# Optimization experiments

Measured on AMD Instinct MI355X. Metric: run time of the kernel, lower is better.

Reference implementation:

```python
import jax, jax.numpy as jnp
import numpy as np

N_CODES = 4096
D = 256


def setup_inputs() -> dict:
    key = jax.random.key(0)
    k_v, k_w = jax.random.split(key)
    v = jax.random.normal(k_v, (8, 2048, D), dtype=jnp.float32)
    # Embedding init ~ N(0,1), then softmax over dim=1, then row 0 set to 1/d (empty feature)
    w = jax.random.normal(k_w, (N_CODES, D), dtype=jnp.float32)
    w = jax.nn.softmax(w, axis=1)
    w = w.at[0].set(1.0 / D)
    return {"v": v, "vectors": w}


def reference(v, vectors):
    n, d = vectors.shape
    cb = vectors[1:]  # exclude the fixed empty feature at index 0
    # ||v - c||^2 = ||v||^2 - 2 v.c + ||c||^2  (avoids [..., n, d] intermediate)
    v2 = jnp.sum(v * v, axis=-1, keepdims=True)              # [..., 1]
    c2 = jnp.sum(cb * cb, axis=-1)                           # [n-1]
    diff = v2 - 2.0 * jnp.einsum('...d,nd->...n', v, cb) + c2  # [..., n-1]
    idx = jnp.argmin(diff, axis=-1) + 1                      # [...]
    # empty-feature mask: any component differs from 1/d
    mask = jnp.any(v != (1.0 / d), axis=-1)
    idx = jnp.where(mask, idx, 0)
    out = vectors[idx]                                       # gather == onehot @ vectors
    loss = jnp.mean(jnp.square(out - jax.lax.stop_gradient(v)))
    used = jnp.array(0, dtype=jnp.int32)  # eval mode: usage pool is empty
    return out, idx, loss, used
```

## Files before the change

kernel.cpp:

```cpp
#include <hip/hip_runtime.h>
#include <hip/hip_fp16.h>
#include <math.h>
#include <stdint.h>


#define M_TOTAL 16384
#define NCODES  4096
#define D_DIM   256

#define OUT_OFF_IDX  (M_TOTAL * D_DIM)
#define OUT_OFF_LOSS (OUT_OFF_IDX + M_TOTAL)

#define VPLANE (M_TOTAL * D_DIM)

typedef _Float16 half8 __attribute__((ext_vector_type(8)));
typedef float    float16v __attribute__((ext_vector_type(16)));

__global__ __launch_bounds__(256) void prep_kernel(
    const float* __restrict__ V, const float* __restrict__ W,
    _Float16* __restrict__ Vhi, _Float16* __restrict__ Vlo,
    _Float16* __restrict__ Bp, float* __restrict__ v2, float* __restrict__ c2,
    uint64_t* __restrict__ pk)
{
  __shared__ float T[16 * 264];
  const int t = threadIdx.x;
  const int rloc = t >> 4, seg = t & 15;
  const bool isW = blockIdx.x < 256;
  const int bid2 = isW ? blockIdx.x : (blockIdx.x - 256);
  const int row = bid2 * 16 + rloc;
  const float* X = isW ? W : V;

  if (!isW && bid2 < 64) pk[bid2 * 256 + t] = ~0ULL;

  const float* src = X + (size_t)row * D_DIM + seg * 16;
  float4 x[4];
#pragma unroll
  for (int u = 0; u < 4; ++u) x[u] = ((const float4*)src)[u];
  union { half8 v; _Float16 e[8]; } uh[2], ul[2];
#pragma unroll
  for (int u = 0; u < 4; ++u) {
    float e4[4] = {x[u].x, x[u].y, x[u].z, x[u].w};
#pragma unroll
    for (int j = 0; j < 4; ++j) {
      const int e = u * 4 + j;
      float s = e4[j] * 1024.0f;
      _Float16 h = (_Float16)s;
      uh[e >> 3].e[e & 7] = h;
      ul[e >> 3].e[e & 7] = (_Float16)(s - (float)h);
    }
    *(float4*)&T[rloc * 264 + seg * 16 + u * 4] = x[u];
  }
  if (isW) {
    const int panel = row >> 5, nin = row & 31;
    _Float16* dst = Bp + ((size_t)panel * 16 + seg) * 2048 + nin * 8;
#pragma unroll
    for (int lh = 0; lh < 2; ++lh) {
      *(half8*)(dst + lh * 256)        = uh[lh].v;
      *(half8*)(dst + 1024 + lh * 256) = ul[lh].v;
    }
  } else {
    _Float16* hd = Vhi + (size_t)row * D_DIM + seg * 16;
    _Float16* ld = Vlo + (size_t)row * D_DIM + seg * 16;
    *(half8*)hd = uh[0].v; *(half8*)(hd + 8) = uh[1].v;
    *(half8*)ld = ul[0].v; *(half8*)(ld + 8) = ul[1].v;
  }
  __syncthreads();
  const int half = (t >> 3) & 1, j = t & 7;
  const float* tr = &T[rloc * 264 + half * 128 + j];
  float r = __fmul_rn(tr[0], tr[0]);
#pragma unroll
  for (int i = 1; i < 16; ++i) { float e = tr[8 * i]; r = __fadd_rn(r, __fmul_rn(e, e)); }
  r = __fadd_rn(r, __shfl_xor(r, 1));
  r = __fadd_rn(r, __shfl_xor(r, 2));
  r = __fadd_rn(r, __shfl_xor(r, 4));
  r = __fadd_rn(r, __shfl_xor(r, 8));
  if ((t & 15) == 0) { if (isW) c2[row] = r; else v2[row] = r; }
}

__global__ __launch_bounds__(256, 2) void vq_mfma_kernel(
    const _Float16* __restrict__ Vhi, const _Float16* __restrict__ Vlo,
    const _Float16* __restrict__ Bp,
    const float* __restrict__ v2, const float* __restrict__ c2,
    uint64_t* __restrict__ pk)
{
  __shared__ __align__(16) char smem_raw[69632];
  _Float16* As = (_Float16*)smem_raw;
  uint64_t* red2 = (uint64_t*)(smem_raw + 65536);

  const int tid  = threadIdx.x;
  const int lane = tid & 63;
  const int wave = tid >> 6;
  const int wr = wave >> 1, wc = wave & 1;
  const int l31 = lane & 31, lhi = lane >> 5;

  const int bid = blockIdx.x;
  const int panel = (bid & 7) * 4 + ((bid >> 3) & 3);
  const int mblk  = bid >> 5;
  const int m0 = mblk * 256;
  const int n0 = panel * 128;
  const int p32 = panel * 4 + wc * 2;

  int src[4], dst[4];
#pragma unroll
  for (int u = 0; u < 4; ++u) {
    const int g = tid + 256 * u, m = g >> 2, kb = g & 3;
    src[u] = (m0 + m) * D_DIM + kb * 8;
    dst[u] = m * 32 + (kb ^ (m & 3)) * 8;
  }

  float16v acc[4][2];
#pragma unroll
  for (int mb = 0; mb < 4; ++mb)
#pragma unroll
    for (int nb = 0; nb < 2; ++nb) acc[mb][nb] = (float16v)0.0f;

  half8 sh[4], sl[4];
#pragma unroll
  for (int u = 0; u < 4; ++u) {
    sh[u] = *(const half8*)(Vhi + src[u]);
    sl[u] = *(const half8*)(Vlo + src[u]);
  }
#pragma unroll
  for (int u = 0; u < 4; ++u) {
    *(half8*)(As + dst[u])        = sh[u];
    *(half8*)(As + 8192 + dst[u]) = sl[u];
  }

  half8 bh[2][2], bl[2][2];
#pragma unroll
  for (int nb = 0; nb < 2; ++nb) {
    const _Float16* bp = Bp + ((size_t)(p32 + nb) * 16) * 2048 + lane * 8;
    bh[0][nb] = *(const half8*)bp;
    bl[0][nb] = *(const half8*)(bp + 1024);
  }
  __syncthreads();

  for (int kt = 0; kt < 8; ++kt) {
    const int cur = kt & 1;
    _Float16* Ac = As + cur * 16384;
    if (kt < 7) {
#pragma unroll
      for (int u = 0; u < 4; ++u) {
        sh[u] = *(const half8*)(Vhi + src[u] + (kt + 1) * 32);
        sl[u] = *(const half8*)(Vlo + src[u] + (kt + 1) * 32);
      }
    }
#pragma unroll
    for (int ks = 0; ks < 2; ++ks) {
      const int kstep = kt * 2 + ks;
      const int pcur = kstep & 1, pnxt = pcur ^ 1;
      if (kstep < 15) {
#pragma unroll
        for (int nb = 0; nb < 2; ++nb) {
          const _Float16* bp = Bp + ((size_t)(p32 + nb) * 16 + kstep + 1) * 2048 + lane * 8;
          bh[pnxt][nb] = *(const half8*)bp;
          bl[pnxt][nb] = *(const half8*)(bp + 1024);
        }
      }
      half8 ah[4], al[4];
#pragma unroll
      for (int mb = 0; mb < 4; ++mb) {
        const int m = wr * 128 + mb * 32 + l31;
        const int c = (ks * 2 + lhi) ^ (m & 3);
        ah[mb] = *(const half8*)(Ac + m * 32 + c * 8);
        al[mb] = *(const half8*)(Ac + 8192 + m * 32 + c * 8);
      }
#pragma unroll
      for (int nb = 0; nb < 2; ++nb)
#pragma unroll
        for (int mb = 0; mb < 4; ++mb)
          acc[mb][nb] = __builtin_amdgcn_mfma_f32_32x32x16_f16(ah[mb], bh[pcur][nb], acc[mb][nb], 0, 0, 0);
#pragma unroll
      for (int nb = 0; nb < 2; ++nb)
#pragma unroll
        for (int mb = 0; mb < 4; ++mb)
          acc[mb][nb] = __builtin_amdgcn_mfma_f32_32x32x16_f16(ah[mb], bl[pcur][nb], acc[mb][nb], 0, 0, 0);
#pragma unroll
      for (int nb = 0; nb < 2; ++nb)
#pragma unroll
        for (int mb = 0; mb < 4; ++mb)
          acc[mb][nb] = __builtin_amdgcn_mfma_f32_32x32x16_f16(al[mb], bh[pcur][nb], acc[mb][nb], 0, 0, 0);
    }
    if (kt < 7) {
      _Float16* An = As + (cur ^ 1) * 16384;
#pragma unroll
      for (int u = 0; u < 4; ++u) {
        *(half8*)(An + dst[u])        = sh[u];
        *(half8*)(An + 8192 + dst[u]) = sl[u];
      }
    }
    __syncthreads();
  }

  float c2r[2];
#pragma unroll
  for (int nb = 0; nb < 2; ++nb) c2r[nb] = c2[n0 + wc * 64 + nb * 32 + l31];

  uint64_t* wbuf = (uint64_t*)smem_raw + wave * 1056;

#pragma unroll
  for (int mb = 0; mb < 4; ++mb) {
#pragma unroll
    for (int r = 0; r < 16; ++r) {
      const int rowin = (r & 3) + 8 * (r >> 2) + 4 * lhi;
      const float v2m = v2[m0 + wr * 128 + mb * 32 + rowin];
      uint64_t b = ~0ULL;
#pragma unroll
      for (int nb = 0; nb < 2; ++nb) {
        const int n = n0 + wc * 64 + nb * 32 + l31;
        float dot = acc[mb][nb][r] * 0x1p-20f;
        float dd  = __fadd_rn(__fsub_rn(v2m, 2.0f * dot), c2r[nb]);
        if (n == 0) dd = INFINITY;
        uint64_t p = ((uint64_t)__float_as_uint(dd) << 32) | (uint32_t)n;
        if (p < b) b = p;
      }
      wbuf[(r * 2 + lhi) * 33 + l31] = b;
    }
    __syncthreads();
    {
      const int f = lane >> 1, hf = lane & 1;
      const uint64_t* rp = wbuf + f * 33 + hf * 16;
      uint64_t m = rp[0];
#pragma unroll
      for (int i = 1; i < 16; ++i) { uint64_t v = rp[i]; if (v < m) m = v; }
      uint64_t o = __shfl_xor((unsigned long long)m, 1);
      if (o < m) m = o;
      if (hf == 0) {
        const int r_ = f >> 1, lh2 = f & 1;
        const int rowin = (r_ & 3) + 8 * (r_ >> 2) + 4 * lh2;
        red2[(wr * 128 + mb * 32 + rowin) * 2 + wc] = m;
      }
    }
    __syncthreads();
  }

  uint64_t a0 = red2[tid * 2], a1 = red2[tid * 2 + 1];
  atomicMin((unsigned long long*)&pk[m0 + tid], (unsigned long long)(a0 < a1 ? a0 : a1));
}

__global__ __launch_bounds__(256) void gather_kernel(
    const float* __restrict__ V, const float* __restrict__ W,
    const uint64_t* __restrict__ pk,
    float* __restrict__ out, float* __restrict__ outIdx,
    float* __restrict__ lossPartial)
{
  const int q = blockIdx.x * 4 + (threadIdx.x >> 6);
  const int l = threadIdx.x & 63;
  const uint64_t b = pk[q];
  float4 vv = *(const float4*)(V + (size_t)q * D_DIM + l * 4);
  const float inv = 0.00390625f;
  bool ne = (vv.x != inv) | (vv.y != inv) | (vv.z != inv) | (vv.w != inv);
  const int idx = __ballot(ne) ? (int)(uint32_t)b : 0;
  float4 o4 = *(const float4*)(W + (size_t)idx * D_DIM + l * 4);
  *(float4*)(out + (size_t)q * D_DIM + l * 4) = o4;
  if (l == 0) outIdx[q] = (float)idx;
  float dx = o4.x - vv.x, dy = o4.y - vv.y, dz = o4.z - vv.z, dw = o4.w - vv.w;
  float s = dx * dx + dy * dy + dz * dz + dw * dw;
#pragma unroll
  for (int off = 32; off; off >>= 1) s += __shfl_xor(s, off);
  if (l == 0) lossPartial[q] = s;
}

__global__ __launch_bounds__(256) void finalize_kernel(
    const float* __restrict__ lossPartial, float* __restrict__ out)
{
  const int t = threadIdx.x;
  __shared__ float red[256];
  float s = 0.0f;
  for (int i = t; i < M_TOTAL; i += 256) s += lossPartial[i];
  red[t] = s;
  __syncthreads();
  for (int st = 128; st > 0; st >>= 1) {
    if (t < st) red[t] += red[t + st];
    __syncthreads();
  }
  if (t == 0) {
    out[0] = (float)((double)red[0] / (double)(M_TOTAL * D_DIM));
    out[1] = 0.0f;
  }
}

extern "C" void kernel_launch(void* const* d_in, const int* in_sizes, int n_in,
                              void* d_out, int out_size, void* d_ws, size_t ws_size,
                              hipStream_t stream) {
  const float* V = (const float*)d_in[0];
  const float* W = (const float*)d_in[1];
  float* out = (float*)d_out;

  _Float16* Vhi = (_Float16*)d_out;
  _Float16* Vlo = Vhi + VPLANE;

  char* ws = (char*)d_ws;
  _Float16* Bp  = (_Float16*)(ws);
  float*    c2  = (float*)(ws + 8388608);
  float*    v2  = (float*)(ws + 8388608 + 16384);
  uint64_t* pk  = (uint64_t*)(ws + 8388608 + 16384 + 65536);
  float* lossPartial = (float*)(ws + 8388608 + 16384 + 65536 + 131072);

  prep_kernel<<<1280, 256, 0, stream>>>(V, W, Vhi, Vlo, Bp, v2, c2, pk);
  vq_mfma_kernel<<<2048, 256, 0, stream>>>(Vhi, Vlo, Bp, v2, c2, pk);
  gather_kernel<<<M_TOTAL / 4, 256, 0, stream>>>(V, W, pk, out, out + OUT_OFF_IDX, lossPartial);
  finalize_kernel<<<1, 256, 0, stream>>>(lossPartial, out + OUT_OFF_LOSS);
}
```

Measured before the change: 204.3 us.

## Stream low-half A fragments from registers, shrink LDS, remap blocks, fuse loss finalize

The low-precision residual of V is now written by prep in an MFMA-fragment-ordered layout and loaded directly into registers per k-step, bypassing LDS. This halves LDS traffic and the LDS footprint, which may allow more resident blocks per CU. The B panel layout is compacted, and the block-to-tile mapping is changed to group M blocks and panels per XCD for better L2 reuse. The separate finalize kernel is replaced by atomic partial sums with a last-block reduction inside gather, which saves one launch but adds atomics and makes the float summation order nondeterministic.

Measured after the change: 297.8 us. +45.8%, slower.

```diff
diff --git a/kernel.cpp b/kernel.cpp
--- a/kernel.cpp
+++ b/kernel.cpp
@@ -18,9 +18,9 @@
 
 __global__ __launch_bounds__(256) void prep_kernel(
     const float* __restrict__ V, const float* __restrict__ W,
-    _Float16* __restrict__ Vhi, _Float16* __restrict__ Vlo,
+    _Float16* __restrict__ Vhi, _Float16* __restrict__ Aplo,
     _Float16* __restrict__ Bp, float* __restrict__ v2, float* __restrict__ c2,
-    uint64_t* __restrict__ pk)
+    uint64_t* __restrict__ pk, float* __restrict__ lossP, int* __restrict__ cnt)
 {
   __shared__ float T[16 * 264];
   const int t = threadIdx.x;
@@ -31,6 +31,7 @@
   const float* X = isW ? W : V;
 
   if (!isW && bid2 < 64) pk[bid2 * 256 + t] = ~0ULL;
+  if (isW && bid2 == 0) { if (t < 64) lossP[t] = 0.0f; if (t == 64) *cnt = 0; }
 
   const float* src = X + (size_t)row * D_DIM + seg * 16;
   float4 x[4];
@@ -52,17 +53,19 @@
   }
   if (isW) {
     const int panel = row >> 5, nin = row & 31;
-    _Float16* dst = Bp + ((size_t)panel * 16 + seg) * 2048 + nin * 8;
+    _Float16* dst = Bp + ((size_t)panel * 16 + seg) * 1024 + nin * 8;
 #pragma unroll
     for (int lh = 0; lh < 2; ++lh) {
-      *(half8*)(dst + lh * 256)        = uh[lh].v;
-      *(half8*)(dst + 1024 + lh * 256) = ul[lh].v;
+      *(half8*)(dst + lh * 256)       = uh[lh].v;
+      *(half8*)(dst + 512 + lh * 256) = ul[lh].v;
     }
   } else {
     _Float16* hd = Vhi + (size_t)row * D_DIM + seg * 16;
-    _Float16* ld = Vlo + (size_t)row * D_DIM + seg * 16;
     *(half8*)hd = uh[0].v; *(half8*)(hd + 8) = uh[1].v;
-    *(half8*)ld = ul[0].v; *(half8*)(ld + 8) = ul[1].v;
+    const int mblk = row >> 8, wrr = (row >> 7) & 1, mbb = (row >> 5) & 3, nl = row & 31;
+    _Float16* ad = Aplo + ((((size_t)mblk * 2 + wrr) * 4 + mbb) * 16 + seg) * 512 + nl * 8;
+    *(half8*)ad        = ul[0].v;
+    *(half8*)(ad + 256) = ul[1].v;
   }
   __syncthreads();
   const int half = (t >> 3) & 1, j = t & 7;
@@ -78,14 +81,14 @@
 }
 
 __global__ __launch_bounds__(256, 2) void vq_mfma_kernel(
-    const _Float16* __restrict__ Vhi, const _Float16* __restrict__ Vlo,
+    const _Float16* __restrict__ Vhi, const _Float16* __restrict__ Aplo,
     const _Float16* __restrict__ Bp,
     const float* __restrict__ v2, const float* __restrict__ c2,
     uint64_t* __restrict__ pk)
 {
-  __shared__ __align__(16) char smem_raw[69632];
+  __shared__ __align__(16) char smem_raw[37888];
   _Float16* As = (_Float16*)smem_raw;
-  uint64_t* red2 = (uint64_t*)(smem_raw + 65536);
+  uint64_t* red2 = (uint64_t*)(smem_raw + 33792);
 
   const int tid  = threadIdx.x;
   const int lane = tid & 63;
@@ -94,8 +97,9 @@
   const int l31 = lane & 31, lhi = lane >> 5;
 
   const int bid = blockIdx.x;
-  const int panel = (bid & 7) * 4 + ((bid >> 3) & 3);
-  const int mblk  = bid >> 5;
+  const int xcd = bid & 7, jj = bid >> 3;
+  const int mblk  = (xcd >> 1) * 16 + (jj & 15);
+  const int panel = (xcd & 1) * 16 + (jj >> 4);
   const int m0 = mblk * 256;
   const int n0 = panel * 128;
   const int p32 = panel * 4 + wc * 2;
@@ -114,36 +118,33 @@
 #pragma unroll
     for (int nb = 0; nb < 2; ++nb) acc[mb][nb] = (float16v)0.0f;
 
-  half8 sh[4], sl[4];
-#pragma unroll
-  for (int u = 0; u < 4; ++u) {
-    sh[u] = *(const half8*)(Vhi + src[u]);
-    sl[u] = *(const half8*)(Vlo + src[u]);
-  }
-#pragma unroll
-  for (int u = 0; u < 4; ++u) {
-    *(half8*)(As + dst[u])        = sh[u];
-    *(half8*)(As + 8192 + dst[u]) = sl[u];
-  }
+  half8 sh[4];
+#pragma unroll
+  for (int u = 0; u < 4; ++u) sh[u] = *(const half8*)(Vhi + src[u]);
+#pragma unroll
+  for (int u = 0; u < 4; ++u) *(half8*)(As + dst[u]) = sh[u];
+
+  const _Float16* abase = Aplo + (((size_t)mblk * 2 + wr) * 4) * 16 * 512 + lane * 8;
+  half8 alp[2][4];
+#pragma unroll
+  for (int mb = 0; mb < 4; ++mb)
+    alp[0][mb] = *(const half8*)(abase + (mb * 16 + 0) * 512);
 
   half8 bh[2][2], bl[2][2];
 #pragma unroll
   for (int nb = 0; nb < 2; ++nb) {
-    const _Float16* bp = Bp + ((size_t)(p32 + nb) * 16) * 2048 + lane * 8;
+    const _Float16* bp = Bp + ((size_t)(p32 + nb) * 16) * 1024 + lane * 8;
     bh[0][nb] = *(const half8*)bp;
-    bl[0][nb] = *(const half8*)(bp + 1024);
+    bl[0][nb] = *(const half8*)(bp + 512);
   }
   __syncthreads();
 
   for (int kt = 0; kt < 8; ++kt) {
     const int cur = kt & 1;
-    _Float16* Ac = As + cur * 16384;
+    const _Float16* Ac = As + cur * 8192;
     if (kt < 7) {
 #pragma unroll
-      for (int u = 0; u < 4; ++u) {
-        sh[u] = *(const half8*)(Vhi + src[u] + (kt + 1) * 32);
-        sl[u] = *(const half8*)(Vlo + src[u] + (kt + 1) * 32);
-      }
+      for (int u = 0; u < 4; ++u) sh[u] = *(const half8*)(Vhi + src[u] + (kt + 1) * 32);
     }
 #pragma unroll
     for (int ks = 0; ks < 2; ++ks) {
@@ -152,18 +153,20 @@
       if (kstep < 15) {
 #pragma unroll
         for (int nb = 0; nb < 2; ++nb) {
-          const _Float16* bp = Bp + ((size_t)(p32 + nb) * 16 + kstep + 1) * 2048 + lane * 8;
+          const _Float16* bp = Bp + ((size_t)(p32 + nb) * 16 + kstep + 1) * 1024 + lane * 8;
           bh[pnxt][nb] = *(const half8*)bp;
-          bl[pnxt][nb] = *(const half8*)(bp + 1024);
+          bl[pnxt][nb] = *(const half8*)(bp + 512);
         }
+#pragma unroll
+        for (int mb = 0; mb < 4; ++mb)
+          alp[pnxt][mb] = *(const half8*)(abase + (mb * 16 + kstep + 1) * 512);
       }
-      half8 ah[4], al[4];
+      half8 ah[4];
 #pragma unroll
       for (int mb = 0; mb < 4; ++mb) {
         const int m = wr * 128 + mb * 32 + l31;
         const int c = (ks * 2 + lhi) ^ (m & 3);
         ah[mb] = *(const half8*)(Ac + m * 32 + c * 8);
-        al[mb] = *(const half8*)(Ac + 8192 + m * 32 + c * 8);
       }
 #pragma unroll
       for (int nb = 0; nb < 2; ++nb)
@@ -179,15 +182,12 @@
       for (int nb = 0; nb < 2; ++nb)
 #pragma unroll
         for (int mb = 0; mb < 4; ++mb)
-          acc[mb][nb] = __builtin_amdgcn_mfma_f32_32x32x16_f16(al[mb], bh[pcur][nb], acc[mb][nb], 0, 0, 0);
+          acc[mb][nb] = __builtin_amdgcn_mfma_f32_32x32x16_f16(alp[pcur][mb], bh[pcur][nb], acc[mb][nb], 0, 0, 0);
     }
     if (kt < 7) {
-      _Float16* An = As + (cur ^ 1) * 16384;
-#pragma unroll
-      for (int u = 0; u < 4; ++u) {
-        *(half8*)(An + dst[u])        = sh[u];
-        *(half8*)(An + 8192 + dst[u]) = sl[u];
-      }
+      _Float16* An = As + (cur ^ 1) * 8192;
+#pragma unroll
+      for (int u = 0; u < 4; ++u) *(half8*)(An + dst[u]) = sh[u];
     }
     __syncthreads();
   }
@@ -242,9 +242,12 @@
     const float* __restrict__ V, const float* __restrict__ W,
     const uint64_t* __restrict__ pk,
     float* __restrict__ out, float* __restrict__ outIdx,
-    float* __restrict__ lossPartial)
+    float* __restrict__ lossP, int* __restrict__ cnt, float* __restrict__ lossOut)
 {
-  const int q = blockIdx.x * 4 + (threadIdx.x >> 6);
+  __shared__ float sred[4];
+  __shared__ int lastFlag;
+  const int wv = threadIdx.x >> 6;
+  const int q = blockIdx.x * 4 + wv;
   const int l = threadIdx.x & 63;
   const uint64_t b = pk[q];
   float4 vv = *(const float4*)(V + (size_t)q * D_DIM + l * 4);
@@ -258,25 +261,24 @@
   float s = dx * dx + dy * dy + dz * dz + dw * dw;
 #pragma unroll
   for (int off = 32; off; off >>= 1) s += __shfl_xor(s, off);
-  if (l == 0) lossPartial[q] = s;
-}
-
-__global__ __launch_bounds__(256) void finalize_kernel(
-    const float* __restrict__ lossPartial, float* __restrict__ out)
-{
-  const int t = threadIdx.x;
-  __shared__ float red[256];
-  float s = 0.0f;
-  for (int i = t; i < M_TOTAL; i += 256) s += lossPartial[i];
-  red[t] = s;
+  if (l == 0) sred[wv] = s;
   __syncthreads();
-  for (int st = 128; st > 0; st >>= 1) {
-    if (t < st) red[t] += red[t + st];
-    __syncthreads();
-  }
-  if (t == 0) {
-    out[0] = (float)((double)red[0] / (double)(M_TOTAL * D_DIM));
-    out[1] = 0.0f;
+  if (threadIdx.x == 0) {
+    float total = sred[0] + sred[1] + sred[2] + sred[3];
+    atomicAdd(&lossP[blockIdx.x & 63], total);
+    __threadfence();
+    int old = atomicAdd(cnt, 1);
+    lastFlag = (old == gridDim.x - 1);
+  }
+  __syncthreads();
+  if (lastFlag && wv == 0) {
+    float p = atomicAdd(&lossP[l], 0.0f);
+#pragma unroll
+    for (int off = 32; off; off >>= 1) p += __shfl_xor(p, off);
+    if (l == 0) {
+      lossOut[0] = (float)((double)p / (double)(M_TOTAL * D_DIM));
+      lossOut[1] = 0.0f;
+    }
   }
 }
 
@@ -287,18 +289,19 @@
   const float* W = (const float*)d_in[1];
   float* out = (float*)d_out;
 
-  _Float16* Vhi = (_Float16*)d_out;
-  _Float16* Vlo = Vhi + VPLANE;
+  _Float16* Vhi  = (_Float16*)d_out;
+  _Float16* Aplo = Vhi + VPLANE;
 
   char* ws = (char*)d_ws;
   _Float16* Bp  = (_Float16*)(ws);
-  float*    c2  = (float*)(ws + 8388608);
-  float*    v2  = (float*)(ws + 8388608 + 16384);
-  uint64_t* pk  = (uint64_t*)(ws + 8388608 + 16384 + 65536);
-  float* lossPartial = (float*)(ws + 8388608 + 16384 + 65536 + 131072);
-
-  prep_kernel<<<1280, 256, 0, stream>>>(V, W, Vhi, Vlo, Bp, v2, c2, pk);
-  vq_mfma_kernel<<<2048, 256, 0, stream>>>(Vhi, Vlo, Bp, v2, c2, pk);
-  gather_kernel<<<M_TOTAL / 4, 256, 0, stream>>>(V, W, pk, out, out + OUT_OFF_IDX, lossPartial);
-  finalize_kernel<<<1, 256, 0, stream>>>(lossPartial, out + OUT_OFF_LOSS);
+  float*    c2  = (float*)(ws + 4194304);
+  float*    v2  = (float*)(ws + 4194304 + 16384);
+  uint64_t* pk  = (uint64_t*)(ws + 4194304 + 16384 + 65536);
+  float*    lossP = (float*)(ws + 4194304 + 16384 + 65536 + 131072);
+  int*      cnt   = (int*)(ws + 4194304 + 16384 + 65536 + 131072 + 256);
+
+  prep_kernel<<<1280, 256, 0, stream>>>(V, W, Vhi, Aplo, Bp, v2, c2, pk, lossP, cnt);
+  vq_mfma_kernel<<<2048, 256, 0, stream>>>(Vhi, Aplo, Bp, v2, c2, pk);
+  gather_kernel<<<M_TOTAL / 4, 256, 0, stream>>>(V, W, pk, out, out + OUT_OFF_IDX, lossP, cnt,
+                                                 out + OUT_OFF_LOSS);
 }
```
